# Optimization experiments

Hardware: AMD Instinct MI355X
Metric: run time of the kernel (lower is better)

The kernel has to match this reference:

```python
import jax, jax.numpy as jnp
import numpy as np

N_EMBD = 1024
N_HEAD = 16
HEAD_DIM = N_EMBD // N_HEAD
EPS = 1e-5


def setup_inputs() -> dict:
    key = jax.random.key(0)
    ks = jax.random.split(key, 12)
    C = N_EMBD
    s = lambda fan_in: 1.0 / np.sqrt(fan_in)
    return {
        "x": jax.random.normal(ks[0], (2, 2048, C), dtype=jnp.float32),
        "ln1_g": jnp.ones((C,), jnp.float32),
        "ln1_b": jnp.zeros((C,), jnp.float32),
        "w_attn": jax.random.normal(ks[1], (C, 3 * C), jnp.float32) * s(C),
        "b_attn": jnp.zeros((3 * C,), jnp.float32),
        "w_proj": jax.random.normal(ks[2], (C, C), jnp.float32) * s(C),
        "b_proj": jnp.zeros((C,), jnp.float32),
        "ln2_g": jnp.ones((C,), jnp.float32),
        "ln2_b": jnp.zeros((C,), jnp.float32),
        "w_fc": jax.random.normal(ks[3], (C, 4 * C), jnp.float32) * s(C),
        "b_fc": jnp.zeros((4 * C,), jnp.float32),
        "w_fc2": jax.random.normal(ks[4], (4 * C, C), jnp.float32) * s(4 * C),
        "b_fc2": jnp.zeros((C,), jnp.float32),
    }


def _layernorm(x, g, b):
    mu = jnp.mean(x, axis=-1, keepdims=True)
    var = jnp.mean(jnp.square(x - mu), axis=-1, keepdims=True)
    return (x - mu) * jax.lax.rsqrt(var + EPS) * g + b


def _attention(x, w_attn, b_attn, w_proj, b_proj):
    B, T, C = x.shape
    qkv = x @ w_attn + b_attn  # [B,T,3C]
    q, k, v = jnp.split(qkv, 3, axis=-1)
    # [B,H,T,D]
    reshape = lambda t: t.reshape(B, T, N_HEAD, HEAD_DIM).transpose(0, 2, 1, 3)
    q, k, v = reshape(q), reshape(k), reshape(v)
    scale = HEAD_DIM ** (-0.5)
    att = jnp.einsum("bhqd,bhkd->bhqk", q, k) * scale  # [B,H,T,T]
    mask = jnp.tril(jnp.ones((T, T), dtype=bool))
    att = jnp.where(mask, att, -jnp.inf)
    att = jax.nn.softmax(att, axis=-1)
    y = jnp.einsum("bhqk,bhkd->bhqd", att, v)
    y = y.transpose(0, 2, 1, 3).reshape(B, T, C)
    return y @ w_proj + b_proj


def _mlp(x, w_fc, b_fc, w_fc2, b_fc2):
    h = jax.nn.gelu(x @ w_fc + b_fc, approximate=False)  # nn.GELU default = exact erf
    return h @ w_fc2 + b_fc2


def reference(x, ln1_g, ln1_b, w_attn, b_attn, w_proj, b_proj,
              ln2_g, ln2_b, w_fc, b_fc, w_fc2, b_fc2):
    x = x + _attention(_layernorm(x, ln1_g, ln1_b), w_attn, b_attn, w_proj, b_proj)
    x = x + _mlp(_layernorm(x, ln2_g, ln2_b), w_fc, b_fc, w_fc2, b_fc2)
    return x
```

## Files before the change

### kernel.cpp

```cpp
#include <hip/hip_runtime.h>
#include <hip/hip_bf16.h>
#include <math.h>

typedef __attribute__((ext_vector_type(8))) __bf16 bf16x8;
typedef __attribute__((ext_vector_type(4))) float floatx4;
typedef __attribute__((ext_vector_type(8))) unsigned short ushort8;

#define C_EMBD 1024
#define T_SEQ 2048
#define NH 16
#define HD 64

#define WAITV(N) asm volatile("s_waitcnt vmcnt(" #N ")" ::: "memory")
#define WAITL(N) asm volatile("s_waitcnt lgkmcnt(" #N ")" ::: "memory")
#define DSR(d, a, OFF) \
  asm volatile("ds_read_b128 %0, %1 offset:" #OFF : "=v"(d) : "v"(a))

static __device__ __forceinline__ unsigned short f2b(float f) {
  __hip_bfloat16 h = __float2bfloat16(f);
  unsigned short u;
  __builtin_memcpy(&u, &h, sizeof(u));
  return u;
}
static __device__ __forceinline__ float b2f(unsigned short u) {
  unsigned int b = ((unsigned int)u) << 16;
  float f;
  __builtin_memcpy(&f, &b, sizeof(f));
  return f;
}

static __device__ __forceinline__ void gload16(const void* g, void* l) {
  __builtin_amdgcn_global_load_lds(
      (__attribute__((address_space(1))) void*)(void*)g,
      (__attribute__((address_space(3))) void*)l, 16, 0, 0);
}

static __device__ __forceinline__ floatx4 mfma_bf16(bf16x8 a, bf16x8 b, floatx4 c) {
  return __builtin_amdgcn_mfma_f32_16x16x32_bf16(a, b, c, 0, 0, 0);
}

static __device__ __forceinline__ unsigned int lds_addr(const void* p) {
  return (unsigned int)(size_t)(__attribute__((address_space(3))) void*)(void*)p;
}

__global__ __launch_bounds__(256) void wtrans(const float* __restrict__ in,
                                              unsigned short* __restrict__ out,
                                              int K, int N) {
  __shared__ float t[32][33];
  int n0 = blockIdx.x * 32, k0 = blockIdx.y * 32;
  int tx = threadIdx.x & 31, ty = threadIdx.x >> 5;
#pragma unroll
  for (int i = 0; i < 4; i++)
    t[ty + i * 8][tx] = in[(size_t)(k0 + ty + i * 8) * N + n0 + tx];
  __syncthreads();
#pragma unroll
  for (int i = 0; i < 4; i++)
    out[(size_t)(n0 + ty + i * 8) * K + k0 + tx] = f2b(t[tx][ty + i * 8]);
}

__global__ __launch_bounds__(256) void ln_fwd(const float* __restrict__ x,
                                              const float* __restrict__ g,
                                              const float* __restrict__ bta,
                                              unsigned short* __restrict__ out) {
  int row = blockIdx.x;
  int t = threadIdx.x;
  const float4* xr = (const float4*)(x + (size_t)row * C_EMBD);
  float4 v = xr[t];
  float s = v.x + v.y + v.z + v.w;
  float ss = v.x * v.x + v.y * v.y + v.z * v.z + v.w * v.w;
#pragma unroll
  for (int m = 1; m < 64; m <<= 1) {
    s += __shfl_xor(s, m, 64);
    ss += __shfl_xor(ss, m, 64);
  }
  __shared__ float ps[8];
  int wv = t >> 6;
  if ((t & 63) == 0) { ps[wv] = s; ps[4 + wv] = ss; }
  __syncthreads();
  s = ps[0] + ps[1] + ps[2] + ps[3];
  ss = ps[4] + ps[5] + ps[6] + ps[7];
  float mu = s * (1.0f / C_EMBD);
  float var = ss * (1.0f / C_EMBD) - mu * mu;
  float rs = rsqrtf(var + 1e-5f);
  float4 gv = ((const float4*)g)[t];
  float4 bv = ((const float4*)bta)[t];
  ushort4 o;
  o.x = f2b((v.x - mu) * rs * gv.x + bv.x);
  o.y = f2b((v.y - mu) * rs * gv.y + bv.y);
  o.z = f2b((v.z - mu) * rs * gv.z + bv.z);
  o.w = f2b((v.w - mu) * rs * gv.w + bv.w);
  *(ushort4*)(out + (size_t)row * C_EMBD + t * 4) = o;
}

template <int EP, int MI>
__global__ __launch_bounds__(256) void gemm_bt(const unsigned short* __restrict__ A,
                                               const unsigned short* __restrict__ Bt,
                                               const float* __restrict__ bias,
                                               const float* __restrict__ res,
                                               void* __restrict__ outv,
                                               unsigned short* __restrict__ vt,
                                               int M, int N, int K) {
  __shared__ __align__(16) unsigned short As[MI * 32 * 32];
  __shared__ __align__(16) unsigned short Bs[128 * 32];
  const int tid = threadIdx.x;
  const int wv = tid >> 6, ln = tid & 63;
  const int quad = ln >> 4, l15 = ln & 15;
  const int wm = wv >> 1, wn = wv & 1;
  const int m0 = blockIdx.y * (MI * 32), n0 = blockIdx.x * 128;

  floatx4 acc[MI][4];
#pragma unroll
  for (int i = 0; i < MI; i++)
#pragma unroll
    for (int j = 0; j < 4; j++) acc[i][j] = (floatx4)0.0f;

  const int rowA = ln >> 2;
  const int koff = (ln & 3) * 8;

  for (int k0 = 0; k0 < K; k0 += 32) {
    if (k0) __syncthreads();
#pragma unroll
    for (int hh = 0; hh < MI / 2; ++hh) {
      int r = hh * 64 + wv * 16 + rowA;
      gload16(A + (size_t)(m0 + r) * K + k0 + koff, &As[(hh * 64 + wv * 16) * 32]);
    }
#pragma unroll
    for (int hh = 0; hh < 2; ++hh) {
      int r = hh * 64 + wv * 16 + rowA;
      gload16(Bt + (size_t)(n0 + r) * K + k0 + koff, &Bs[(hh * 64 + wv * 16) * 32]);
    }
    __syncthreads();
    bf16x8 af[MI], bfr[4];
#pragma unroll
    for (int mi = 0; mi < MI; mi++)
      af[mi] = *(const bf16x8*)&As[(wm * (MI * 16) + mi * 16 + l15) * 32 + quad * 8];
#pragma unroll
    for (int ni = 0; ni < 4; ni++)
      bfr[ni] = *(const bf16x8*)&Bs[(wn * 64 + ni * 16 + l15) * 32 + quad * 8];
#pragma unroll
    for (int mi = 0; mi < MI; mi++)
#pragma unroll
      for (int ni = 0; ni < 4; ni++)
        acc[mi][ni] = mfma_bf16(af[mi], bfr[ni], acc[mi][ni]);
  }

#pragma unroll
  for (int mi = 0; mi < MI; mi++) {
#pragma unroll
    for (int ni = 0; ni < 4; ni++) {
      int col = n0 + wn * 64 + ni * 16 + l15;
      int rowb = m0 + wm * (MI * 16) + mi * 16 + quad * 4;
      float bc = bias[col];
      if (EP == 1) {
#pragma unroll
        for (int r = 0; r < 4; r++) {
          size_t idx = (size_t)(rowb + r) * N + col;
          ((float*)outv)[idx] = acc[mi][ni][r] + bc + res[idx];
        }
      }
    }
  }
}

template <int EP>
__global__ __launch_bounds__(512, 2) void gemm256(
    const unsigned short* __restrict__ A, const unsigned short* __restrict__ Bt,
    const float* __restrict__ bias, const float* __restrict__ res,
    void* __restrict__ outv, unsigned short* __restrict__ vt,
    float* __restrict__ p0, float* __restrict__ p12,
    int M, int N, int ldK, int KCH) {
  __shared__ __align__(16) unsigned short As[2][16384];
  __shared__ __align__(16) unsigned short Bs[2][16384];
  const int tid = threadIdx.x;
  const int wv = tid >> 6, ln = tid & 63;
  const int quad = ln >> 4, l15 = ln & 15;
  const int wm = wv >> 2, wn = wv & 3;

  const int gx = gridDim.x;
  const int nwg = gx * gridDim.y;
  int id = blockIdx.y * gx + blockIdx.x;
  const int cpx = nwg >> 3;
  id = (id & 7) * cpx + (id >> 3);
  const int n0 = (id % gx) * 256;
  const int m0 = (id / gx) * 256;
  const int bz = blockIdx.z;

  A += (size_t)bz * KCH;
  Bt += (size_t)bz * KCH;

  const unsigned short* aSt =
      A + (size_t)(m0 + wv * 8 + (ln >> 3)) * ldK + (((ln & 7) ^ (ln >> 3)) * 8);
  const unsigned short* bSt =
      Bt + (size_t)(n0 + wv * 8 + (ln >> 3)) * ldK + (((ln & 7) ^ (ln >> 3)) * 8);
  const size_t gstep = (size_t)64 * ldK;

  const int sw0 = ((quad) ^ (l15 & 7)) * 16;
  const int sw1 = ((4 + quad) ^ (l15 & 7)) * 16;
  const unsigned int aoff0 = lds_addr(&As[0][0]) + (wm * 128 + l15) * 128 + sw0;
  const unsigned int aoff1 = lds_addr(&As[0][0]) + (wm * 128 + l15) * 128 + sw1;
  const unsigned int boff0 = lds_addr(&Bs[0][0]) + (wn * 64 + l15) * 128 + sw0;
  const unsigned int boff1 = lds_addr(&Bs[0][0]) + (wn * 64 + l15) * 128 + sw1;

  floatx4 acc[8][4];
#pragma unroll
  for (int i = 0; i < 8; i++)
#pragma unroll
    for (int j = 0; j < 4; j++) acc[i][j] = (floatx4)0.0f;

  const int NT = KCH >> 6;

  auto stA1 = [&](int bi, int kt, int g) {
    gload16(aSt + (size_t)kt * 64 + (size_t)g * gstep,
            &As[bi][(g * 64 + wv * 8) * 64]);
  };
  auto stB1 = [&](int bi, int kt, int g) {
    gload16(bSt + (size_t)kt * 64 + (size_t)g * gstep,
            &Bs[bi][(g * 64 + wv * 8) * 64]);
  };

  stB1(0, 0, 0); stB1(0, 0, 1); stB1(0, 0, 2); stB1(0, 0, 3);
  stA1(0, 0, 0); stA1(0, 0, 2); stA1(0, 0, 1); stA1(0, 0, 3);

  for (int t = 0; t < NT; ++t) {
    const int cur = t & 1;
    const bool more = (t + 1 < NT);
    WAITV(2);
    __builtin_amdgcn_s_barrier();

    const unsigned int ab0 = aoff0 + (cur << 15), ab1 = aoff1 + (cur << 15);
    const unsigned int bb0 = boff0 + (cur << 15), bb1 = boff1 + (cur << 15);
    bf16x8 bf0[4], bf1[4], af0[4], af1[4];
    DSR(bf0[0], bb0, 0);    DSR(bf0[1], bb0, 2048);
    DSR(bf0[2], bb0, 4096); DSR(bf0[3], bb0, 6144);
    DSR(bf1[0], bb1, 0);    DSR(bf1[1], bb1, 2048);
    DSR(bf1[2], bb1, 4096); DSR(bf1[3], bb1, 6144);
    DSR(af0[0], ab0, 0);    DSR(af0[1], ab0, 2048);
    DSR(af0[2], ab0, 4096); DSR(af0[3], ab0, 6144);
    DSR(af1[0], ab1, 0);    DSR(af1[1], ab1, 2048);
    DSR(af1[2], ab1, 4096); DSR(af1[3], ab1, 6144);
    if (more) {
      stB1(cur ^ 1, t + 1, 0); stB1(cur ^ 1, t + 1, 1);
      stB1(cur ^ 1, t + 1, 2); stB1(cur ^ 1, t + 1, 3);
    }
    WAITL(0);
    __builtin_amdgcn_sched_barrier(0);
    __builtin_amdgcn_s_setprio(1);
#pragma unroll
    for (int mi = 0; mi < 4; mi++)
#pragma unroll
      for (int ni = 0; ni < 4; ni++) {
        acc[mi][ni] = mfma_bf16(af0[mi], bf0[ni], acc[mi][ni]);
        acc[mi][ni] = mfma_bf16(af1[mi], bf1[ni], acc[mi][ni]);
      }
    __builtin_amdgcn_s_setprio(0);

    if (more) WAITV(4); else WAITV(0);
    DSR(af0[0], ab0, 8192);  DSR(af0[1], ab0, 10240);
    DSR(af0[2], ab0, 12288); DSR(af0[3], ab0, 14336);
    DSR(af1[0], ab1, 8192);  DSR(af1[1], ab1, 10240);
    DSR(af1[2], ab1, 12288); DSR(af1[3], ab1, 14336);
    if (more) {
      stA1(cur ^ 1, t + 1, 0); stA1(cur ^ 1, t + 1, 2);
      stA1(cur ^ 1, t + 1, 1); stA1(cur ^ 1, t + 1, 3);
    }
    WAITL(0);
    __builtin_amdgcn_sched_barrier(0);
    __builtin_amdgcn_s_setprio(1);
#pragma unroll
    for (int mi = 0; mi < 4; mi++)
#pragma unroll
      for (int ni = 0; ni < 4; ni++) {
        acc[4 + mi][ni] = mfma_bf16(af0[mi], bf0[ni], acc[4 + mi][ni]);
        acc[4 + mi][ni] = mfma_bf16(af1[mi], bf1[ni], acc[4 + mi][ni]);
      }
    __builtin_amdgcn_s_setprio(0);
  }

#pragma unroll
  for (int mi = 0; mi < 8; mi++) {
#pragma unroll
    for (int ni = 0; ni < 4; ni++) {
      const int col = n0 + wn * 64 + ni * 16 + l15;
      const int rowb = m0 + wm * 128 + mi * 16 + quad * 4;
      const float bc = bias ? bias[col] : 0.0f;
      if (EP == 1) {
#pragma unroll
        for (int r = 0; r < 4; r++) {
          size_t idx = (size_t)(rowb + r) * N + col;
          ((float*)outv)[idx] = acc[mi][ni][r] + bc + res[idx];
        }
      } else if (EP == 2) {
#pragma unroll
        for (int r = 0; r < 4; r++) {
          float v = acc[mi][ni][r] + bc;
          v = 0.5f * v * (1.0f + erff(v * 0.70710678118f));
          ((unsigned short*)outv)[(size_t)(rowb + r) * N + col] = f2b(v);
        }
      } else if (EP == 3) {
        if (col < 2048) {
#pragma unroll
          for (int r = 0; r < 4; r++)
            ((unsigned short*)outv)[(size_t)(rowb + r) * N + col] =
                f2b(acc[mi][ni][r] + bc);
        } else {
          int dall = col - 2048;
          int hh2 = dall >> 6, dd = dall & 63;
          int bq = rowb >> 11, t0 = rowb & 2047;
          __align__(8) unsigned short pk[4];
#pragma unroll
          for (int r = 0; r < 4; r++) pk[r] = f2b(acc[mi][ni][r] + bc);
          *(ushort4*)&vt[(size_t)((bq * NH + hh2) * HD + dd) * T_SEQ + t0] =
              *(const ushort4*)pk;
        }
      } else {
        if (bz == 3) {
#pragma unroll
          for (int r = 0; r < 4; r++) {
            size_t idx = (size_t)(rowb + r) * N + col;
            ((float*)outv)[idx] = acc[mi][ni][r] + bc + res[idx];
          }
        } else {
          const size_t MN = (size_t)M * N;
          float* pp = (bz == 0) ? p0 : p12 + (size_t)(bz - 1) * MN;
#pragma unroll
          for (int r = 0; r < 4; r++)
            pp[(size_t)(rowb + r) * N + col] = acc[mi][ni][r];
        }
      }
    }
  }
}

__global__ __launch_bounds__(256) void red3(const float* __restrict__ p0,
                                            const float* __restrict__ p12,
                                            float* __restrict__ out) {
  const size_t MN4 = (size_t)4096 * 1024 / 4;
  for (size_t i = (size_t)blockIdx.x * 256 + threadIdx.x; i < MN4;
       i += (size_t)gridDim.x * 256) {
    float4 a = ((const float4*)p0)[i];
    float4 b = ((const float4*)p12)[i];
    float4 c = ((const float4*)p12)[i + MN4];
    float4 o = ((float4*)out)[i];
    o.x += a.x + b.x + c.x;
    o.y += a.y + b.y + c.y;
    o.z += a.z + b.z + c.z;
    o.w += a.w + b.w + c.w;
    ((float4*)out)[i] = o;
  }
}

__global__ __launch_bounds__(256) void attn_fwd(const unsigned short* __restrict__ qkv,
                                                const unsigned short* __restrict__ vt,
                                                unsigned short* __restrict__ y) {
  __shared__ __align__(16) unsigned short Ks[3][64 * 64];
  __shared__ __align__(16) unsigned short Vs[3][64 * 64];
  __shared__ __align__(16) unsigned short Ps[4 * 16 * 72];
  const int tid = threadIdx.x;
  const int wv = tid >> 6, ln = tid & 63;
  const int quad = ln >> 4, l15 = ln & 15;
  const int pair = blockIdx.x, h = blockIdx.y, b = blockIdx.z;
  unsigned short* Pw = &Ps[wv * 16 * 72];

  const unsigned short* kbase = qkv + (size_t)b * T_SEQ * 3072 + 1024 + h * HD;
  const unsigned short* vbase = vt + (size_t)(b * NH + h) * HD * T_SEQ;

  int koffs[2], voffs[2], ldst[2];
#pragma unroll
  for (int g = 0; g < 2; g++) {
    int S = wv * 128 + g * 64 + ln;
    int r = S >> 3;
    int c = (S & 7) ^ (r & 7);
    koffs[g] = r * 3072 + c * 8;
    voffs[g] = r * T_SEQ + c * 8;
    ldst[g] = wv * 1024 + g * 512;
  }

  auto stage = [&](int kt, int slot) {
#pragma unroll
    for (int g = 0; g < 2; g++) {
      gload16(kbase + (size_t)(kt * 64) * 3072 + koffs[g], &Ks[slot][ldst[g]]);
      gload16(vbase + kt * 64 + voffs[g], &Vs[slot][ldst[g]]);
    }
  };

  for (int ph = 0; ph < 2; ++ph) {
    const int qt = ph ? (31 - pair) : pair;
    const unsigned short* qp =
        qkv + (size_t)(b * T_SEQ + qt * 64 + wv * 16 + l15) * 3072 + h * HD;
    bf16x8 qf[2];
#pragma unroll
    for (int kc = 0; kc < 2; kc++) {
      ushort8 u = *(const ushort8*)(qp + kc * 32 + quad * 8);
      union { ushort8 u; bf16x8 v; } cv;
#pragma unroll
      for (int j = 0; j < 8; j++) cv.u[j] = f2b(b2f(u[j]) * 0.18033688f);
      qf[kc] = cv.v;
    }

    floatx4 o[4];
#pragma unroll
    for (int dt = 0; dt < 4; dt++) o[dt] = (floatx4)0.0f;
    float lacc = 0.0f;

    stage(0, 0);
    if (qt >= 1) stage(1, 1);

    for (int kt = 0; kt <= qt; ++kt) {
      const int slot = kt % 3;
      const bool diag = (kt == qt);
      if (kt < qt) WAITV(4); else WAITV(0);
      __builtin_amdgcn_s_barrier();
      if (kt + 2 <= qt) stage(kt + 2, (kt + 2) % 3);

      const unsigned short* Kc = Ks[slot];
      const unsigned short* Vc = Vs[slot];
      floatx4 s[4];
#pragma unroll
      for (int nt = 0; nt < 4; nt++) s[nt] = (floatx4)0.0f;
#pragma unroll
      for (int nt = 0; nt < 4; nt++)
#pragma unroll
        for (int kc = 0; kc < 2; kc++) {
          bf16x8 kf = *(const bf16x8*)
              &Kc[(nt * 16 + l15) * 64 + (((kc * 4 + quad) ^ (l15 & 7)) * 8)];
          s[nt] = mfma_bf16(kf, qf[kc], s[nt]);
        }

      float psum = 0.0f;
#pragma unroll
      for (int nt = 0; nt < 4; nt++) {
        __align__(8) unsigned short pk[4];
#pragma unroll
        for (int r = 0; r < 4; r++) {
          float sv = s[nt][r];
          if (diag && (nt * 16 + quad * 4 + r > wv * 16 + l15)) sv = -1e30f;
          float p = exp2f(sv - 12.0f);
          psum += p;
          pk[r] = f2b(p);
        }
        *(ushort4*)&Pw[l15 * 72 + nt * 16 + quad * 4] = *(const ushort4*)pk;
      }
      lacc += psum;

      bf16x8 pf0 = *(const bf16x8*)&Pw[l15 * 72 + quad * 8];
      bf16x8 pf1 = *(const bf16x8*)&Pw[l15 * 72 + 32 + quad * 8];
#pragma unroll
      for (int dt = 0; dt < 4; dt++) {
        bf16x8 vf0 = *(const bf16x8*)
            &Vc[(dt * 16 + l15) * 64 + ((quad ^ (l15 & 7)) * 8)];
        bf16x8 vf1 = *(const bf16x8*)
            &Vc[(dt * 16 + l15) * 64 + (((4 + quad) ^ (l15 & 7)) * 8)];
        o[dt] = mfma_bf16(vf0, pf0, o[dt]);
        o[dt] = mfma_bf16(vf1, pf1, o[dt]);
      }
    }

    lacc += __shfl_xor(lacc, 16, 64);
    lacc += __shfl_xor(lacc, 32, 64);
    float rinv = 1.0f / lacc;
#pragma unroll
    for (int dt = 0; dt < 4; dt++) {
      __align__(8) unsigned short ov[4];
#pragma unroll
      for (int r = 0; r < 4; r++) ov[r] = f2b(o[dt][r] * rinv);
      *(ushort4*)&y[(size_t)(b * T_SEQ + qt * 64 + wv * 16 + l15) * C_EMBD +
                    h * HD + dt * 16 + quad * 4] = *(const ushort4*)ov;
    }
  }
}

extern "C" void kernel_launch(void* const* d_in, const int* in_sizes, int n_in,
                              void* d_out, int out_size, void* d_ws, size_t ws_size,
                              hipStream_t stream) {
  (void)in_sizes; (void)n_in; (void)out_size; (void)ws_size;
  const float* x      = (const float*)d_in[0];
  const float* ln1_g  = (const float*)d_in[1];
  const float* ln1_b  = (const float*)d_in[2];
  const float* w_attn = (const float*)d_in[3];
  const float* b_attn = (const float*)d_in[4];
  const float* w_proj = (const float*)d_in[5];
  const float* b_proj = (const float*)d_in[6];
  const float* ln2_g  = (const float*)d_in[7];
  const float* ln2_b  = (const float*)d_in[8];
  const float* w_fc   = (const float*)d_in[9];
  const float* b_fc   = (const float*)d_in[10];
  const float* w_fc2  = (const float*)d_in[11];
  const float* b_fc2  = (const float*)d_in[12];
  float* out = (float*)d_out;

  char* wsb = (char*)d_ws;
  char* ws = wsb;
  unsigned short* wat  = (unsigned short*)ws; ws += (size_t)3072 * 1024 * 2;
  unsigned short* wpt  = (unsigned short*)ws; ws += (size_t)1024 * 1024 * 2;
  unsigned short* wft  = (unsigned short*)ws; ws += (size_t)4096 * 1024 * 2;
  unsigned short* wf2t = (unsigned short*)ws; ws += (size_t)1024 * 4096 * 2;
  unsigned short* xn   = (unsigned short*)ws; ws += (size_t)4096 * 1024 * 2;
  unsigned short* qkv  = (unsigned short*)ws; ws += (size_t)4096 * 3072 * 2;
  unsigned short* yat  = (unsigned short*)ws; ws += (size_t)4096 * 1024 * 2;
  unsigned short* hbuf = (unsigned short*)ws; ws += (size_t)4096 * 4096 * 2;
  unsigned short* vt = hbuf;
  float* p0  = (float*)wsb;
  float* p12 = (float*)(wsb + (size_t)24 * 1024 * 1024);

  wtrans<<<dim3(3072 / 32, 1024 / 32), 256, 0, stream>>>(w_attn, wat, 1024, 3072);
  wtrans<<<dim3(1024 / 32, 1024 / 32), 256, 0, stream>>>(w_proj, wpt, 1024, 1024);
  wtrans<<<dim3(4096 / 32, 1024 / 32), 256, 0, stream>>>(w_fc, wft, 1024, 4096);
  wtrans<<<dim3(1024 / 32, 4096 / 32), 256, 0, stream>>>(w_fc2, wf2t, 4096, 1024);

  ln_fwd<<<4096, 256, 0, stream>>>(x, ln1_g, ln1_b, xn);
  gemm256<3><<<dim3(3072 / 256, 4096 / 256), 512, 0, stream>>>(
      xn, wat, b_attn, nullptr, qkv, vt, nullptr, nullptr, 4096, 3072, 1024, 1024);
  attn_fwd<<<dim3(16, NH, 2), 256, 0, stream>>>(qkv, vt, yat);
  gemm_bt<1, 2><<<dim3(8, 64), 256, 0, stream>>>(
      yat, wpt, b_proj, x, out, nullptr, 4096, 1024, 1024);
  ln_fwd<<<4096, 256, 0, stream>>>(out, ln2_g, ln2_b, xn);
  gemm256<2><<<dim3(4096 / 256, 4096 / 256), 512, 0, stream>>>(
      xn, wft, b_fc, nullptr, hbuf, nullptr, nullptr, nullptr, 4096, 4096, 1024, 1024);
  gemm256<4><<<dim3(1024 / 256, 4096 / 256, 4), 512, 0, stream>>>(
      hbuf, wf2t, b_fc2, out, out, nullptr, p0, p12, 4096, 1024, 4096, 1024);
  red3<<<2048, 256, 0, stream>>>(p0, p12, out);
}
```

Baseline: 368.8 us.

## Split GEMM K-step into four barrier-synchronised MFMA phases with staged A/B prefetch

Restructures the GEMM main loop from two compute halves into four smaller phases, each loading only two A row-fragments, with extra workgroup barriers between phases so waves stay in lockstep (ping-pong style). Global prefetch of the next A tile is issued in phase one and of B in phase two, and the loop now waits for all outstanding global loads (vmcnt 0) at the top of each iteration. The aim is to reduce register pressure and interleave LDS reads, global loads and MFMA work more evenly across waves. In exchange it adds many s_barrier calls per iteration and a stricter wait, which could stall the pipeline.

```diff
diff --git a/kernel.cpp b/kernel.cpp
--- a/kernel.cpp
+++ b/kernel.cpp
@@ -218,62 +218,104 @@
             &Bs[bi][(g * 64 + wv * 8) * 64]);
   };
 
+  stA1(0, 0, 0); stA1(0, 0, 1); stA1(0, 0, 2); stA1(0, 0, 3);
   stB1(0, 0, 0); stB1(0, 0, 1); stB1(0, 0, 2); stB1(0, 0, 3);
-  stA1(0, 0, 0); stA1(0, 0, 2); stA1(0, 0, 1); stA1(0, 0, 3);
 
   for (int t = 0; t < NT; ++t) {
     const int cur = t & 1;
     const bool more = (t + 1 < NT);
-    WAITV(2);
-    __builtin_amdgcn_s_barrier();
-
     const unsigned int ab0 = aoff0 + (cur << 15), ab1 = aoff1 + (cur << 15);
     const unsigned int bb0 = boff0 + (cur << 15), bb1 = boff1 + (cur << 15);
-    bf16x8 bf0[4], bf1[4], af0[4], af1[4];
-    DSR(bf0[0], bb0, 0);    DSR(bf0[1], bb0, 2048);
-    DSR(bf0[2], bb0, 4096); DSR(bf0[3], bb0, 6144);
-    DSR(bf1[0], bb1, 0);    DSR(bf1[1], bb1, 2048);
-    DSR(bf1[2], bb1, 4096); DSR(bf1[3], bb1, 6144);
-    DSR(af0[0], ab0, 0);    DSR(af0[1], ab0, 2048);
-    DSR(af0[2], ab0, 4096); DSR(af0[3], ab0, 6144);
-    DSR(af1[0], ab1, 0);    DSR(af1[1], ab1, 2048);
-    DSR(af1[2], ab1, 4096); DSR(af1[3], ab1, 6144);
-    if (more) {
-      stB1(cur ^ 1, t + 1, 0); stB1(cur ^ 1, t + 1, 1);
-      stB1(cur ^ 1, t + 1, 2); stB1(cur ^ 1, t + 1, 3);
-    }
-    WAITL(0);
-    __builtin_amdgcn_sched_barrier(0);
-    __builtin_amdgcn_s_setprio(1);
-#pragma unroll
-    for (int mi = 0; mi < 4; mi++)
+
+    WAITV(0);
+    __builtin_amdgcn_s_barrier();
+
+    bf16x8 bf0[4], bf1[4];
+    {
+      bf16x8 a0, a1, a2, a3;
+      DSR(bf0[0], bb0, 0);    DSR(bf0[1], bb0, 2048);
+      DSR(bf0[2], bb0, 4096); DSR(bf0[3], bb0, 6144);
+      DSR(bf1[0], bb1, 0);    DSR(bf1[1], bb1, 2048);
+      DSR(bf1[2], bb1, 4096); DSR(bf1[3], bb1, 6144);
+      DSR(a0, ab0, 0); DSR(a1, ab0, 2048);
+      DSR(a2, ab1, 0); DSR(a3, ab1, 2048);
+      if (more) {
+        stA1(cur ^ 1, t + 1, 0); stA1(cur ^ 1, t + 1, 1);
+        stA1(cur ^ 1, t + 1, 2); stA1(cur ^ 1, t + 1, 3);
+      }
+      WAITL(8);
+      __builtin_amdgcn_s_barrier();
+      WAITL(0);
+      __builtin_amdgcn_sched_barrier(0);
+      __builtin_amdgcn_s_setprio(1);
 #pragma unroll
       for (int ni = 0; ni < 4; ni++) {
-        acc[mi][ni] = mfma_bf16(af0[mi], bf0[ni], acc[mi][ni]);
-        acc[mi][ni] = mfma_bf16(af1[mi], bf1[ni], acc[mi][ni]);
-      }
-    __builtin_amdgcn_s_setprio(0);
-
-    if (more) WAITV(4); else WAITV(0);
-    DSR(af0[0], ab0, 8192);  DSR(af0[1], ab0, 10240);
-    DSR(af0[2], ab0, 12288); DSR(af0[3], ab0, 14336);
-    DSR(af1[0], ab1, 8192);  DSR(af1[1], ab1, 10240);
-    DSR(af1[2], ab1, 12288); DSR(af1[3], ab1, 14336);
-    if (more) {
-      stA1(cur ^ 1, t + 1, 0); stA1(cur ^ 1, t + 1, 2);
-      stA1(cur ^ 1, t + 1, 1); stA1(cur ^ 1, t + 1, 3);
-    }
-    WAITL(0);
-    __builtin_amdgcn_sched_barrier(0);
-    __builtin_amdgcn_s_setprio(1);
-#pragma unroll
-    for (int mi = 0; mi < 4; mi++)
+        acc[0][ni] = mfma_bf16(a0, bf0[ni], acc[0][ni]);
+        acc[0][ni] = mfma_bf16(a2, bf1[ni], acc[0][ni]);
+        acc[1][ni] = mfma_bf16(a1, bf0[ni], acc[1][ni]);
+        acc[1][ni] = mfma_bf16(a3, bf1[ni], acc[1][ni]);
+      }
+      __builtin_amdgcn_s_setprio(0);
+      __builtin_amdgcn_s_barrier();
+    }
+    {
+      bf16x8 a0, a1, a2, a3;
+      DSR(a0, ab0, 4096); DSR(a1, ab0, 6144);
+      DSR(a2, ab1, 4096); DSR(a3, ab1, 6144);
+      if (more) {
+        stB1(cur ^ 1, t + 1, 0); stB1(cur ^ 1, t + 1, 1);
+        stB1(cur ^ 1, t + 1, 2); stB1(cur ^ 1, t + 1, 3);
+      }
+      __builtin_amdgcn_s_barrier();
+      WAITL(0);
+      __builtin_amdgcn_sched_barrier(0);
+      __builtin_amdgcn_s_setprio(1);
 #pragma unroll
       for (int ni = 0; ni < 4; ni++) {
-        acc[4 + mi][ni] = mfma_bf16(af0[mi], bf0[ni], acc[4 + mi][ni]);
-        acc[4 + mi][ni] = mfma_bf16(af1[mi], bf1[ni], acc[4 + mi][ni]);
-      }
-    __builtin_amdgcn_s_setprio(0);
+        acc[2][ni] = mfma_bf16(a0, bf0[ni], acc[2][ni]);
+        acc[2][ni] = mfma_bf16(a2, bf1[ni], acc[2][ni]);
+        acc[3][ni] = mfma_bf16(a1, bf0[ni], acc[3][ni]);
+        acc[3][ni] = mfma_bf16(a3, bf1[ni], acc[3][ni]);
+      }
+      __builtin_amdgcn_s_setprio(0);
+      __builtin_amdgcn_s_barrier();
+    }
+    {
+      bf16x8 a0, a1, a2, a3;
+      DSR(a0, ab0, 8192); DSR(a1, ab0, 10240);
+      DSR(a2, ab1, 8192); DSR(a3, ab1, 10240);
+      __builtin_amdgcn_s_barrier();
+      WAITL(0);
+      __builtin_amdgcn_sched_barrier(0);
+      __builtin_amdgcn_s_setprio(1);
+#pragma unroll
+      for (int ni = 0; ni < 4; ni++) {
+        acc[4][ni] = mfma_bf16(a0, bf0[ni], acc[4][ni]);
+        acc[4][ni] = mfma_bf16(a2, bf1[ni], acc[4][ni]);
+        acc[5][ni] = mfma_bf16(a1, bf0[ni], acc[5][ni]);
+        acc[5][ni] = mfma_bf16(a3, bf1[ni], acc[5][ni]);
+      }
+      __builtin_amdgcn_s_setprio(0);
+      __builtin_amdgcn_s_barrier();
+    }
+    {
+      bf16x8 a0, a1, a2, a3;
+      DSR(a0, ab0, 12288); DSR(a1, ab0, 14336);
+      DSR(a2, ab1, 12288); DSR(a3, ab1, 14336);
+      __builtin_amdgcn_s_barrier();
+      WAITL(0);
+      __builtin_amdgcn_sched_barrier(0);
+      __builtin_amdgcn_s_setprio(1);
+#pragma unroll
+      for (int ni = 0; ni < 4; ni++) {
+        acc[6][ni] = mfma_bf16(a0, bf0[ni], acc[6][ni]);
+        acc[6][ni] = mfma_bf16(a2, bf1[ni], acc[6][ni]);
+        acc[7][ni] = mfma_bf16(a1, bf0[ni], acc[7][ni]);
+        acc[7][ni] = mfma_bf16(a3, bf1[ni], acc[7][ni]);
+      }
+      __builtin_amdgcn_s_setprio(0);
+      __builtin_amdgcn_s_barrier();
+    }
   }
 
 #pragma unroll
```

After: 377.6 us. +2.4%, slower.

## Replace 256x256 GEMM with 128x128 tile kernel for all projections

Applied to the files above, without the earlier changes.

The 512-thread 256x256-tile GEMM becomes a 256-thread 128x128-tile GEMM, and every linear layer uses it, including the output projection that previously ran a simple single-buffered gemm_bt kernel. Smaller tiles give more workgroups (more than the CU count for the 1024-wide GEMMs) and smaller LDS use, addressing low occupancy and tail effects. The prefetch now issues all A and B loads up front and waits vmcnt(0) each iteration, which gives up some load/compute overlap. Smaller tiles also mean less data reuse per tile and more global traffic.

```diff
diff --git a/kernel.cpp b/kernel.cpp
--- a/kernel.cpp
+++ b/kernel.cpp
@@ -92,97 +92,27 @@
   *(ushort4*)(out + (size_t)row * C_EMBD + t * 4) = o;
 }
 
-template <int EP, int MI>
-__global__ __launch_bounds__(256) void gemm_bt(const unsigned short* __restrict__ A,
-                                               const unsigned short* __restrict__ Bt,
-                                               const float* __restrict__ bias,
-                                               const float* __restrict__ res,
-                                               void* __restrict__ outv,
-                                               unsigned short* __restrict__ vt,
-                                               int M, int N, int K) {
-  __shared__ __align__(16) unsigned short As[MI * 32 * 32];
-  __shared__ __align__(16) unsigned short Bs[128 * 32];
-  const int tid = threadIdx.x;
-  const int wv = tid >> 6, ln = tid & 63;
-  const int quad = ln >> 4, l15 = ln & 15;
-  const int wm = wv >> 1, wn = wv & 1;
-  const int m0 = blockIdx.y * (MI * 32), n0 = blockIdx.x * 128;
-
-  floatx4 acc[MI][4];
-#pragma unroll
-  for (int i = 0; i < MI; i++)
-#pragma unroll
-    for (int j = 0; j < 4; j++) acc[i][j] = (floatx4)0.0f;
-
-  const int rowA = ln >> 2;
-  const int koff = (ln & 3) * 8;
-
-  for (int k0 = 0; k0 < K; k0 += 32) {
-    if (k0) __syncthreads();
-#pragma unroll
-    for (int hh = 0; hh < MI / 2; ++hh) {
-      int r = hh * 64 + wv * 16 + rowA;
-      gload16(A + (size_t)(m0 + r) * K + k0 + koff, &As[(hh * 64 + wv * 16) * 32]);
-    }
-#pragma unroll
-    for (int hh = 0; hh < 2; ++hh) {
-      int r = hh * 64 + wv * 16 + rowA;
-      gload16(Bt + (size_t)(n0 + r) * K + k0 + koff, &Bs[(hh * 64 + wv * 16) * 32]);
-    }
-    __syncthreads();
-    bf16x8 af[MI], bfr[4];
-#pragma unroll
-    for (int mi = 0; mi < MI; mi++)
-      af[mi] = *(const bf16x8*)&As[(wm * (MI * 16) + mi * 16 + l15) * 32 + quad * 8];
-#pragma unroll
-    for (int ni = 0; ni < 4; ni++)
-      bfr[ni] = *(const bf16x8*)&Bs[(wn * 64 + ni * 16 + l15) * 32 + quad * 8];
-#pragma unroll
-    for (int mi = 0; mi < MI; mi++)
-#pragma unroll
-      for (int ni = 0; ni < 4; ni++)
-        acc[mi][ni] = mfma_bf16(af[mi], bfr[ni], acc[mi][ni]);
-  }
-
-#pragma unroll
-  for (int mi = 0; mi < MI; mi++) {
-#pragma unroll
-    for (int ni = 0; ni < 4; ni++) {
-      int col = n0 + wn * 64 + ni * 16 + l15;
-      int rowb = m0 + wm * (MI * 16) + mi * 16 + quad * 4;
-      float bc = bias[col];
-      if (EP == 1) {
-#pragma unroll
-        for (int r = 0; r < 4; r++) {
-          size_t idx = (size_t)(rowb + r) * N + col;
-          ((float*)outv)[idx] = acc[mi][ni][r] + bc + res[idx];
-        }
-      }
-    }
-  }
-}
-
 template <int EP>
-__global__ __launch_bounds__(512, 2) void gemm256(
+__global__ __launch_bounds__(256, 2) void gemm128(
     const unsigned short* __restrict__ A, const unsigned short* __restrict__ Bt,
     const float* __restrict__ bias, const float* __restrict__ res,
     void* __restrict__ outv, unsigned short* __restrict__ vt,
     float* __restrict__ p0, float* __restrict__ p12,
     int M, int N, int ldK, int KCH) {
-  __shared__ __align__(16) unsigned short As[2][16384];
-  __shared__ __align__(16) unsigned short Bs[2][16384];
+  __shared__ __align__(16) unsigned short As[2][8192];
+  __shared__ __align__(16) unsigned short Bs[2][8192];
   const int tid = threadIdx.x;
   const int wv = tid >> 6, ln = tid & 63;
   const int quad = ln >> 4, l15 = ln & 15;
-  const int wm = wv >> 2, wn = wv & 3;
+  const int wm = wv >> 1, wn = wv & 1;
 
   const int gx = gridDim.x;
   const int nwg = gx * gridDim.y;
   int id = blockIdx.y * gx + blockIdx.x;
   const int cpx = nwg >> 3;
   id = (id & 7) * cpx + (id >> 3);
-  const int n0 = (id % gx) * 256;
-  const int m0 = (id / gx) * 256;
+  const int n0 = (id % gx) * 128;
+  const int m0 = (id / gx) * 128;
   const int bz = blockIdx.z;
 
   A += (size_t)bz * KCH;
@@ -192,18 +122,18 @@
       A + (size_t)(m0 + wv * 8 + (ln >> 3)) * ldK + (((ln & 7) ^ (ln >> 3)) * 8);
   const unsigned short* bSt =
       Bt + (size_t)(n0 + wv * 8 + (ln >> 3)) * ldK + (((ln & 7) ^ (ln >> 3)) * 8);
-  const size_t gstep = (size_t)64 * ldK;
+  const size_t gstep = (size_t)32 * ldK;
 
   const int sw0 = ((quad) ^ (l15 & 7)) * 16;
   const int sw1 = ((4 + quad) ^ (l15 & 7)) * 16;
-  const unsigned int aoff0 = lds_addr(&As[0][0]) + (wm * 128 + l15) * 128 + sw0;
-  const unsigned int aoff1 = lds_addr(&As[0][0]) + (wm * 128 + l15) * 128 + sw1;
+  const unsigned int aoff0 = lds_addr(&As[0][0]) + (wm * 64 + l15) * 128 + sw0;
+  const unsigned int aoff1 = lds_addr(&As[0][0]) + (wm * 64 + l15) * 128 + sw1;
   const unsigned int boff0 = lds_addr(&Bs[0][0]) + (wn * 64 + l15) * 128 + sw0;
   const unsigned int boff1 = lds_addr(&Bs[0][0]) + (wn * 64 + l15) * 128 + sw1;
 
-  floatx4 acc[8][4];
-#pragma unroll
-  for (int i = 0; i < 8; i++)
+  floatx4 acc[4][4];
+#pragma unroll
+  for (int i = 0; i < 4; i++)
 #pragma unroll
     for (int j = 0; j < 4; j++) acc[i][j] = (floatx4)0.0f;
 
@@ -211,77 +141,71 @@
 
   auto stA1 = [&](int bi, int kt, int g) {
     gload16(aSt + (size_t)kt * 64 + (size_t)g * gstep,
-            &As[bi][(g * 64 + wv * 8) * 64]);
+            &As[bi][(g * 32 + wv * 8) * 64]);
   };
   auto stB1 = [&](int bi, int kt, int g) {
     gload16(bSt + (size_t)kt * 64 + (size_t)g * gstep,
-            &Bs[bi][(g * 64 + wv * 8) * 64]);
+            &Bs[bi][(g * 32 + wv * 8) * 64]);
   };
 
   stB1(0, 0, 0); stB1(0, 0, 1); stB1(0, 0, 2); stB1(0, 0, 3);
-  stA1(0, 0, 0); stA1(0, 0, 2); stA1(0, 0, 1); stA1(0, 0, 3);
+  stA1(0, 0, 0); stA1(0, 0, 1); stA1(0, 0, 2); stA1(0, 0, 3);
 
   for (int t = 0; t < NT; ++t) {
     const int cur = t & 1;
     const bool more = (t + 1 < NT);
-    WAITV(2);
+    const unsigned int ab0 = aoff0 + (cur << 14), ab1 = aoff1 + (cur << 14);
+    const unsigned int bb0 = boff0 + (cur << 14), bb1 = boff1 + (cur << 14);
+
+    WAITV(0);
     __builtin_amdgcn_s_barrier();
 
-    const unsigned int ab0 = aoff0 + (cur << 15), ab1 = aoff1 + (cur << 15);
-    const unsigned int bb0 = boff0 + (cur << 15), bb1 = boff1 + (cur << 15);
-    bf16x8 bf0[4], bf1[4], af0[4], af1[4];
+    bf16x8 bf0[4], bf1[4], a0, a1, a2, a3;
     DSR(bf0[0], bb0, 0);    DSR(bf0[1], bb0, 2048);
     DSR(bf0[2], bb0, 4096); DSR(bf0[3], bb0, 6144);
     DSR(bf1[0], bb1, 0);    DSR(bf1[1], bb1, 2048);
     DSR(bf1[2], bb1, 4096); DSR(bf1[3], bb1, 6144);
-    DSR(af0[0], ab0, 0);    DSR(af0[1], ab0, 2048);
-    DSR(af0[2], ab0, 4096); DSR(af0[3], ab0, 6144);
-    DSR(af1[0], ab1, 0);    DSR(af1[1], ab1, 2048);
-    DSR(af1[2], ab1, 4096); DSR(af1[3], ab1, 6144);
+    DSR(a0, ab0, 0); DSR(a1, ab0, 2048);
+    DSR(a2, ab1, 0); DSR(a3, ab1, 2048);
     if (more) {
       stB1(cur ^ 1, t + 1, 0); stB1(cur ^ 1, t + 1, 1);
       stB1(cur ^ 1, t + 1, 2); stB1(cur ^ 1, t + 1, 3);
+      stA1(cur ^ 1, t + 1, 0); stA1(cur ^ 1, t + 1, 1);
+      stA1(cur ^ 1, t + 1, 2); stA1(cur ^ 1, t + 1, 3);
     }
     WAITL(0);
     __builtin_amdgcn_sched_barrier(0);
     __builtin_amdgcn_s_setprio(1);
 #pragma unroll
-    for (int mi = 0; mi < 4; mi++)
-#pragma unroll
-      for (int ni = 0; ni < 4; ni++) {
-        acc[mi][ni] = mfma_bf16(af0[mi], bf0[ni], acc[mi][ni]);
-        acc[mi][ni] = mfma_bf16(af1[mi], bf1[ni], acc[mi][ni]);
-      }
+    for (int ni = 0; ni < 4; ni++) {
+      acc[0][ni] = mfma_bf16(a0, bf0[ni], acc[0][ni]);
+      acc[0][ni] = mfma_bf16(a2, bf1[ni], acc[0][ni]);
+      acc[1][ni] = mfma_bf16(a1, bf0[ni], acc[1][ni]);
+      acc[1][ni] = mfma_bf16(a3, bf1[ni], acc[1][ni]);
+    }
     __builtin_amdgcn_s_setprio(0);
 
-    if (more) WAITV(4); else WAITV(0);
-    DSR(af0[0], ab0, 8192);  DSR(af0[1], ab0, 10240);
-    DSR(af0[2], ab0, 12288); DSR(af0[3], ab0, 14336);
-    DSR(af1[0], ab1, 8192);  DSR(af1[1], ab1, 10240);
-    DSR(af1[2], ab1, 12288); DSR(af1[3], ab1, 14336);
-    if (more) {
-      stA1(cur ^ 1, t + 1, 0); stA1(cur ^ 1, t + 1, 2);
-      stA1(cur ^ 1, t + 1, 1); stA1(cur ^ 1, t + 1, 3);
-    }
+    DSR(a0, ab0, 4096); DSR(a1, ab0, 6144);
+    DSR(a2, ab1, 4096); DSR(a3, ab1, 6144);
     WAITL(0);
     __builtin_amdgcn_sched_barrier(0);
     __builtin_amdgcn_s_setprio(1);
 #pragma unroll
-    for (int mi = 0; mi < 4; mi++)
-#pragma unroll
-      for (int ni = 0; ni < 4; ni++) {
-        acc[4 + mi][ni] = mfma_bf16(af0[mi], bf0[ni], acc[4 + mi][ni]);
-        acc[4 + mi][ni] = mfma_bf16(af1[mi], bf1[ni], acc[4 + mi][ni]);
-      }
+    for (int ni = 0; ni < 4; ni++) {
+      acc[2][ni] = mfma_bf16(a0, bf0[ni], acc[2][ni]);
+      acc[2][ni] = mfma_bf16(a2, bf1[ni], acc[2][ni]);
+      acc[3][ni] = mfma_bf16(a1, bf0[ni], acc[3][ni]);
+      acc[3][ni] = mfma_bf16(a3, bf1[ni], acc[3][ni]);
+    }
     __builtin_amdgcn_s_setprio(0);
   }
 
 #pragma unroll
-  for (int mi = 0; mi < 8; mi++) {
+  for (int mi = 0; mi < 4; mi++) {
 #pragma unroll
     for (int ni = 0; ni < 4; ni++) {
       const int col = n0 + wn * 64 + ni * 16 + l15;
-      const int rowb = m0 + wm * 128 + mi * 16 + quad * 4;
+      const int rowb = m0 + wm * 64 + mi * 16 + quad * 4;
       const float bc = bias ? bias[col] : 0.0f;
       if (EP == 1) {
 #pragma unroll
@@ -508,15 +432,15 @@
   wtrans<<<dim3(1024 / 32, 4096 / 32), 256, 0, stream>>>(w_fc2, wf2t, 4096, 1024);
 
   ln_fwd<<<4096, 256, 0, stream>>>(x, ln1_g, ln1_b, xn);
-  gemm256<3><<<dim3(3072 / 256, 4096 / 256), 512, 0, stream>>>(
+  gemm128<3><<<dim3(3072 / 128, 4096 / 128), 256, 0, stream>>>(
       xn, wat, b_attn, nullptr, qkv, vt, nullptr, nullptr, 4096, 3072, 1024, 1024);
   attn_fwd<<<dim3(16, NH, 2), 256, 0, stream>>>(qkv, vt, yat);
-  gemm_bt<1, 2><<<dim3(8, 64), 256, 0, stream>>>(
-      yat, wpt, b_proj, x, out, nullptr, 4096, 1024, 1024);
+  gemm128<1><<<dim3(1024 / 128, 4096 / 128), 256, 0, stream>>>(
+      yat, wpt, b_proj, x, out, nullptr, nullptr, nullptr, 4096, 1024, 1024, 1024);
   ln_fwd<<<4096, 256, 0, stream>>>(out, ln2_g, ln2_b, xn);
-  gemm256<2><<<dim3(4096 / 256, 4096 / 256), 512, 0, stream>>>(
+  gemm128<2><<<dim3(4096 / 128, 4096 / 128), 256, 0, stream>>>(
       xn, wft, b_fc, nullptr, hbuf, nullptr, nullptr, nullptr, 4096, 4096, 1024, 1024);
-  gemm256<4><<<dim3(1024 / 256, 4096 / 256, 4), 512, 0, stream>>>(
+  gemm128<4><<<dim3(1024 / 128, 4096 / 128, 4), 256, 0, stream>>>(
       hbuf, wf2t, b_fc2, out, out, nullptr, p0, p12, 4096, 1024, 4096, 1024);
   red3<<<2048, 256, 0, stream>>>(p0, p12, out);
 }
```

After: 367.9 us. No clear change (-0.2%).
